# Optimization experiments

Hardware: AMD Instinct MI355X
Metric: run time of the kernel (lower is better)

## Reference

```python
import jax, jax.numpy as jnp
import numpy as np

HIDDEN = 1024
NUM_HEADS = 16
HEAD_DIM = HIDDEN // NUM_HEADS  # 64
MLP_HIDDEN = 4096
RMS_EPS = 1e-6


def setup_inputs() -> dict:
    key = jax.random.key(0)
    ks = jax.random.split(key, 4)
    B, L = 2, 2048
    x = jax.random.normal(ks[0], (B, L, HIDDEN), dtype=jnp.float32)
    pe = jax.random.normal(ks[1], (1, 1, L, HEAD_DIM // 2, 2, 2), dtype=jnp.float32)
    W1 = jax.random.normal(ks[2], (HIDDEN, 3 * HIDDEN + MLP_HIDDEN), dtype=jnp.float32) * (HIDDEN ** -0.5)
    b1 = jnp.zeros((3 * HIDDEN + MLP_HIDDEN,), dtype=jnp.float32)
    W2 = jax.random.normal(ks[3], (HIDDEN + MLP_HIDDEN, HIDDEN), dtype=jnp.float32) * ((HIDDEN + MLP_HIDDEN) ** -0.5)
    b2 = jnp.zeros((HIDDEN,), dtype=jnp.float32)
    q_scale = jnp.ones((HEAD_DIM,), dtype=jnp.float32)
    k_scale = jnp.ones((HEAD_DIM,), dtype=jnp.float32)
    return {"x": x, "pe": pe, "W1": W1, "b1": b1, "W2": W2, "b2": b2,
            "q_scale": q_scale, "k_scale": k_scale}


def _rms_norm(t, scale):
    # RMSNorm over last dim (head_dim) with learnable scale (flux QKNorm)
    rrms = jax.lax.rsqrt(jnp.mean(jnp.square(t), axis=-1, keepdims=True) + RMS_EPS)
    return t * rrms * scale


def _apply_rope(xq, xk, pe):
    # pe: [1,1,L,D/2,2,2]; x*: [B,H,L,D]
    def rope(t):
        t_ = t.reshape(*t.shape[:-1], -1, 1, 2)  # [B,H,L,D/2,1,2]
        out = pe[..., 0] * t_[..., 0] + pe[..., 1] * t_[..., 1]  # [B,H,L,D/2,2]
        return out.reshape(*t.shape)
    return rope(xq), rope(xk)


def reference(x, pe, W1, b1, W2, b2, q_scale, k_scale):
    B, L, _ = x.shape
    h = x @ W1 + b1  # [B,L,3H+Mh]
    qkv, mlp = h[..., : 3 * HIDDEN], h[..., 3 * HIDDEN:]
    # 'B L (K H D) -> K B H L D'
    qkv = qkv.reshape(B, L, 3, NUM_HEADS, HEAD_DIM).transpose(2, 0, 3, 1, 4)
    q, k, v = qkv[0], qkv[1], qkv[2]
    q = _rms_norm(q, q_scale)
    k = _rms_norm(k, k_scale)
    q, k = _apply_rope(q, k, pe)
    scale = HEAD_DIM ** -0.5
    scores = jnp.einsum('bhqd,bhkd->bhqk', q, k) * scale
    attn = jnp.einsum('bhqk,bhkd->bhqd', jax.nn.softmax(scores, axis=-1), v)
    attn = attn.transpose(0, 2, 1, 3).reshape(B, L, HIDDEN)  # 'B H L D -> B L (H D)'
    out = jnp.concatenate((attn, jax.nn.gelu(mlp)), axis=2) @ W2 + b2
    return out
```

## Files before the change

kernel.cpp:

```cpp
#include <hip/hip_runtime.h>

typedef __bf16 bf16;
typedef __bf16 bf16x8 __attribute__((ext_vector_type(8)));
typedef float f32x4 __attribute__((ext_vector_type(4)));
typedef float f32x16 __attribute__((ext_vector_type(16)));

#define GLDS16(gp, lp) __builtin_amdgcn_global_load_lds( \
    (__attribute__((address_space(1))) void*)(gp), \
    (__attribute__((address_space(3))) void*)(lp), 16, 0, 0)

__device__ inline float ex2(float x) { return exp2f(x); }

__device__ inline float gelu_fast(float x) {
    float t = ex2(-2.3022081702f * (x + 0.044715f * x * x * x));
    return x * __builtin_amdgcn_rcpf(1.0f + t);
}


__global__ void f2b_kernel(const float* __restrict__ src, bf16* __restrict__ dst, long n) {
    long i = ((long)blockIdx.x * 256 + threadIdx.x) * 4;
    if (i + 3 < n) {
        float4 v = *(const float4*)&src[i];
        dst[i + 0] = (bf16)v.x;
        dst[i + 1] = (bf16)v.y;
        dst[i + 2] = (bf16)v.z;
        dst[i + 3] = (bf16)v.w;
    }
}

__global__ __launch_bounds__(256) void transpose_f2b(const float* __restrict__ W,
                                                     bf16* __restrict__ WT,
                                                     int K, int N) {
    __shared__ float tile[32][33];
    int tx = threadIdx.x & 31;
    int ty = threadIdx.x >> 5;
    int n0 = blockIdx.x * 32;
    int k0 = blockIdx.y * 32;
#pragma unroll
    for (int i = 0; i < 4; ++i)
        tile[ty + i * 8][tx] = W[(long)(k0 + ty + i * 8) * N + n0 + tx];
    __syncthreads();
#pragma unroll
    for (int i = 0; i < 4; ++i)
        WT[(long)(n0 + ty + i * 8) * K + k0 + tx] = (bf16)tile[tx][ty + i * 8];
}

template <int EPI>
__global__ __launch_bounds__(256) void gemm_bt(const bf16* __restrict__ A,
                                               const bf16* __restrict__ BT,
                                               const float* __restrict__ bias,
                                               void* __restrict__ C0,
                                               void* __restrict__ C1,
                                               int M, int N, int K, int kch) {
    __shared__ bf16 Asm[128 * 32];
    __shared__ bf16 Bsm[128 * 32];
    int tid = threadIdx.x;
    int w = tid >> 6, l = tid & 63;
    int wr = w >> 1, wc = w & 1;
    int bm = blockIdx.x * 128;
    int bn = blockIdx.y * 128;
    int k0base = (EPI == 1) ? blockIdx.z * kch : 0;

    f32x4 acc[4][4] = {};

    int arow = l >> 2;
    int acol = (l & 3) * 8;
    int fr = l & 15;
    int fk = (l >> 4) * 8;

    int nk = kch >> 5;
    for (int kt = 0; kt < nk; ++kt) {
        int k0 = k0base + kt * 32;
#pragma unroll
        for (int it = 0; it < 2; ++it) {
            int c = it * 4 + w;
            const bf16* ga = A + (long)(bm + c * 16 + arow) * K + k0 + acol;
            GLDS16(ga, &Asm[c * 512]);
            const bf16* gb = BT + (long)(bn + c * 16 + arow) * K + k0 + acol;
            GLDS16(gb, &Bsm[c * 512]);
        }
        asm volatile("s_waitcnt vmcnt(0)" ::: "memory");
        __syncthreads();

        bf16x8 af[4], bfr[4];
#pragma unroll
        for (int m = 0; m < 4; ++m)
            af[m] = *(const bf16x8*)&Asm[(wr * 64 + m * 16 + fr) * 32 + fk];
#pragma unroll
        for (int n = 0; n < 4; ++n)
            bfr[n] = *(const bf16x8*)&Bsm[(wc * 64 + n * 16 + fr) * 32 + fk];
#pragma unroll
        for (int m = 0; m < 4; ++m)
#pragma unroll
            for (int n = 0; n < 4; ++n)
                acc[m][n] = __builtin_amdgcn_mfma_f32_16x16x32_bf16(af[m], bfr[n], acc[m][n], 0, 0, 0);
        __syncthreads();
    }

    int orow0 = bm + wr * 64;
    int ocol0 = bn + wc * 64;
    if (EPI == 0) {
        bf16* hp = (bf16*)C0;
        bf16* cat = (bf16*)C1;
        bool gel = (bn >= 3072);
#pragma unroll
        for (int m = 0; m < 4; ++m) {
            int row = orow0 + m * 16 + (l >> 4) * 4;
#pragma unroll
            for (int n = 0; n < 4; ++n) {
                int col = ocol0 + n * 16 + (l & 15);
                float bv = bias[col];
#pragma unroll
                for (int r = 0; r < 4; ++r) {
                    float v = acc[m][n][r] + bv;
                    if (gel) {
                        cat[(long)(row + r) * 5120 + 1024 + col - 3072] = (bf16)gelu_fast(v);
                    } else {
                        hp[(long)(row + r) * N + col] = (bf16)v;
                    }
                }
            }
        }
    } else {
        float* cz = (float*)C0 + (long)blockIdx.z * M * N;
#pragma unroll
        for (int m = 0; m < 4; ++m) {
            int row = orow0 + m * 16 + (l >> 4) * 4;
#pragma unroll
            for (int n = 0; n < 4; ++n) {
                int col = ocol0 + n * 16 + (l & 15);
#pragma unroll
                for (int r = 0; r < 4; ++r)
                    cz[(long)(row + r) * N + col] = acc[m][n][r];
            }
        }
    }
}

__global__ __launch_bounds__(256) void reduce4_kernel(const float* __restrict__ part,
                                                      const float* __restrict__ b2,
                                                      float* __restrict__ out) {
    const long stride4 = 4096L * 1024 / 4;
#pragma unroll
    for (int it = 0; it < 2; ++it) {
        long i4 = (long)blockIdx.x * 512 + it * 256 + threadIdx.x;
        float4 s = *(const float4*)&b2[(i4 * 4) & 1023];
        const float4* p = (const float4*)part;
#pragma unroll
        for (int z = 0; z < 4; ++z) {
            float4 v = p[z * stride4 + i4];
            s.x += v.x; s.y += v.y; s.z += v.z; s.w += v.w;
        }
        *(float4*)&out[i4 * 4] = s;
    }
}

__global__ __launch_bounds__(256) void qkv_kernel(const bf16* __restrict__ h,
                                                  const float* __restrict__ pe,
                                                  const float* __restrict__ qsc_,
                                                  const float* __restrict__ ksc_,
                                                  bf16* __restrict__ qo,
                                                  bf16* __restrict__ ko) {
    int t = blockIdx.x;
    int b = t >> 11;
    int lpos = t & 2047;
    int wv = threadIdx.x >> 6;
    int d = threadIdx.x & 63;
    const bf16* hrow = h + (long)t * 7168;
    float pe0 = pe[lpos * 128 + (d >> 1) * 4 + (d & 1) * 2 + 0];
    float pe1 = pe[lpos * 128 + (d >> 1) * 4 + (d & 1) * 2 + 1];
    float qsc = qsc_[d], ksc = ksc_[d];
#pragma unroll 1
    for (int it = 0; it < 4; ++it) {
        int hh = wv * 4 + it;
        float qv = (float)hrow[hh * 64 + d];
        float kv = (float)hrow[1024 + hh * 64 + d];
        float ssq = qv * qv, ssk = kv * kv;
#pragma unroll
        for (int off = 1; off < 64; off <<= 1) {
            ssq += __shfl_xor(ssq, off, 64);
            ssk += __shfl_xor(ssk, off, 64);
        }
        float qn = qv * rsqrtf(ssq * (1.0f / 64.0f) + 1e-6f) * qsc;
        float kn = kv * rsqrtf(ssk * (1.0f / 64.0f) + 1e-6f) * ksc;
        float qe = __shfl(qn, d & 62, 64), qodd = __shfl(qn, d | 1, 64);
        float ke = __shfl(kn, d & 62, 64), kodd = __shfl(kn, d | 1, 64);
        float qr = (pe0 * qe + pe1 * qodd) * 0.18033688011112042f;
        float kr = pe0 * ke + pe1 * kodd;
        long base = ((long)(b * 16 + hh) * 2048 + lpos) * 64 + d;
        qo[base] = (bf16)qr;
        ko[base] = (bf16)kr;
    }
}

__global__ __launch_bounds__(256) void vtrans_kernel(const bf16* __restrict__ h,
                                                     bf16* __restrict__ vT) {
    __shared__ unsigned short tile[64 * 65];
    int bh = blockIdx.x;
    int b = bh >> 4, hh = bh & 15;
    int l0 = blockIdx.y * 64;
    int tid = threadIdx.x;

    int r = tid >> 3, c = tid & 7;
#pragma unroll
    for (int p = 0; p < 2; ++p) {
        int row = r + p * 32;
        const bf16* src = h + (long)(b * 2048 + l0 + row) * 7168 + 2048 + hh * 64 + c * 8;
        bf16x8 v = *(const bf16x8*)src;
        union { bf16x8 v; unsigned short s[8]; } u; u.v = v;
#pragma unroll
        for (int e = 0; e < 8; ++e) tile[row * 65 + c * 8 + e] = u.s[e];
    }
    __syncthreads();
#pragma unroll
    for (int p = 0; p < 2; ++p) {
        int idx = tid + p * 256;
        int d = idx >> 3, kg = idx & 7;
        union { bf16x8 v; unsigned short s[8]; } u;
#pragma unroll
        for (int e = 0; e < 8; ++e) u.s[e] = tile[(kg * 8 + e) * 65 + d];
        *(bf16x8*)&vT[((long)bh * 64 + d) * 2048 + l0 + kg * 8] = u.v;
    }
}

__global__ __launch_bounds__(512) void attn_kernel(const bf16* __restrict__ qg,
                                                   const bf16* __restrict__ kg_,
                                                   const bf16* __restrict__ vT,
                                                   bf16* __restrict__ cat) {
    __shared__ __align__(16) char lds[65536];
    char* Kl0 = lds;
    char* Kl1 = lds + 8192;
    char* Vl0 = lds + 16384;
    char* Vl1 = lds + 24576;

    int bidx = blockIdx.x;
    int bh = bidx & 31;
    int qblk = bidx >> 5;
    int b = bh >> 4, hh = bh & 15;
    int tid = threadIdx.x;
    int wv = tid >> 6, l = tid & 63;
    int h = l >> 5, ln = l & 31;
    int sw = (ln & 7) << 4;

    char* Pw = lds + 32768 + wv * 4096;

    const bf16* qbase = qg + ((long)bh * 2048 + qblk * 256 + wv * 32 + ln) * 64 + h * 8;
    bf16x8 qf[4];
#pragma unroll
    for (int ds = 0; ds < 4; ++ds) qf[ds] = *(const bf16x8*)(qbase + ds * 16);

    f32x16 Oa0 = {}, Oa1 = {};
    float m = -1e30f, lsum = 0.0f;

    int kr = tid >> 3, kg = tid & 7;
    int swb = (kg * 16) ^ ((kr & 7) << 4);
    const bf16* gK = kg_ + ((long)bh * 2048 + kr) * 64 + kg * 8;
    const bf16* gV = vT + ((long)bh * 64 + kr) * 2048 + kg * 8;

    bf16x8 rk = *(const bf16x8*)gK;
    bf16x8 rv = *(const bf16x8*)gV;
    *(bf16x8*)(Kl0 + kr * 128 + swb) = rk;
    *(bf16x8*)(Vl0 + kr * 128 + swb) = rv;
    __syncthreads();

    int c = 0;
    for (int t = 0; t < 32; ++t) {
        if (t < 31) {
            rk = *(const bf16x8*)(gK + (long)(t + 1) * 4096);
            rv = *(const bf16x8*)(gV + (t + 1) * 64);
        }
        const char* Kc = c ? Kl1 : Kl0;
        const char* Vc = c ? Vl1 : Vl0;

        f32x16 S0 = {}, S1 = {};
        __builtin_amdgcn_s_setprio(1);
#pragma unroll
        for (int ds = 0; ds < 4; ++ds) {
            bf16x8 kf0 = *(const bf16x8*)(Kc + ln * 128 + ((ds * 32 + h * 16) ^ sw));
            bf16x8 kf1 = *(const bf16x8*)(Kc + (32 + ln) * 128 + ((ds * 32 + h * 16) ^ sw));
            S0 = __builtin_amdgcn_mfma_f32_32x32x16_bf16(kf0, qf[ds], S0, 0, 0, 0);
            S1 = __builtin_amdgcn_mfma_f32_32x32x16_bf16(kf1, qf[ds], S1, 0, 0, 0);
        }
        __builtin_amdgcn_s_setprio(0);

        float tmax = S0[0];
#pragma unroll
        for (int r = 1; r < 16; ++r) tmax = fmaxf(tmax, S0[r]);
#pragma unroll
        for (int r = 0; r < 16; ++r) tmax = fmaxf(tmax, S1[r]);
        tmax = fmaxf(tmax, __shfl_xor(tmax, 32, 64));

        if (!__all(tmax - m <= 8.0f)) {
            float mn = fmaxf(m, tmax);
            float es = ex2(m - mn);
            lsum *= es;
            m = mn;
#pragma unroll
            for (int r = 0; r < 16; ++r) {
                int rowq = (r & 3) + 8 * (r >> 2) + 4 * h;
                float esr = __shfl(es, rowq, 64);
                Oa0[r] *= esr;
                Oa1[r] *= esr;
            }
        }

        float ps = 0.0f;
#pragma unroll
        for (int kvt = 0; kvt < 2; ++kvt) {
            float p[16];
#pragma unroll
            for (int r = 0; r < 16; ++r) {
                float v = ex2((kvt ? S1[r] : S0[r]) - m);
                p[r] = v;
                ps += v;
            }
#pragma unroll
            for (int i = 0; i < 8; ++i) {
                union { bf16 bb[2]; unsigned u; } pr;
                pr.bb[0] = (bf16)p[2 * i];
                pr.bb[1] = (bf16)p[2 * i + 1];
                int kv = ((2 * i) & 3) + 8 * (i >> 1) + 4 * h + 32 * kvt;
                *(unsigned*)(Pw + ln * 128 + ((kv * 2) ^ sw)) = pr.u;
            }
        }
        lsum += ps + __shfl_xor(ps, 32, 64);

        asm volatile("s_waitcnt lgkmcnt(0)" ::: "memory");

        bf16x8 pa[4];
#pragma unroll
        for (int s = 0; s < 4; ++s)
            pa[s] = *(const bf16x8*)(Pw + ln * 128 + ((s * 32 + h * 16) ^ sw));

        __builtin_amdgcn_s_setprio(1);
#pragma unroll
        for (int s = 0; s < 4; ++s) {
            bf16x8 vf0 = *(const bf16x8*)(Vc + ln * 128 + ((s * 32 + h * 16) ^ sw));
            bf16x8 vf1 = *(const bf16x8*)(Vc + (32 + ln) * 128 + ((s * 32 + h * 16) ^ sw));
            Oa0 = __builtin_amdgcn_mfma_f32_32x32x16_bf16(pa[s], vf0, Oa0, 0, 0, 0);
            Oa1 = __builtin_amdgcn_mfma_f32_32x32x16_bf16(pa[s], vf1, Oa1, 0, 0, 0);
        }
        __builtin_amdgcn_s_setprio(0);

        __syncthreads();
        if (t < 31) {
            char* Kn = c ? Kl0 : Kl1;
            char* Vn = c ? Vl0 : Vl1;
            *(bf16x8*)(Kn + kr * 128 + swb) = rk;
            *(bf16x8*)(Vn + kr * 128 + swb) = rv;
        }
        __syncthreads();
        c ^= 1;
    }

#pragma unroll
    for (int r = 0; r < 16; ++r) {
        int rowq = (r & 3) + 8 * (r >> 2) + 4 * h;
        float ls = __shfl(lsum, rowq, 64);
        float inv = 1.0f / ls;
        long trow = (long)b * 2048 + qblk * 256 + wv * 32 + rowq;
        cat[trow * 5120 + hh * 64 + ln] = (bf16)(Oa0[r] * inv);
        cat[trow * 5120 + hh * 64 + 32 + ln] = (bf16)(Oa1[r] * inv);
    }
}


extern "C" void kernel_launch(void* const* d_in, const int* in_sizes, int n_in,
                              void* d_out, int out_size, void* d_ws, size_t ws_size,
                              hipStream_t stream) {
    const float* x  = (const float*)d_in[0];
    const float* pe = (const float*)d_in[1];
    const float* W1 = (const float*)d_in[2];
    const float* b1 = (const float*)d_in[3];
    const float* W2 = (const float*)d_in[4];
    const float* b2 = (const float*)d_in[5];
    const float* qs = (const float*)d_in[6];
    const float* ks = (const float*)d_in[7];
    float* out = (float*)d_out;

    char* ws = (char*)d_ws;
    bf16* xb  = (bf16*)(ws);
    bf16* w1t = (bf16*)(ws + 8388608);
    bf16* w2t = (bf16*)(ws + 23068672);
    bf16* h   = (bf16*)(ws + 33554432);
    bf16* qb  = (bf16*)(ws + 92274688);
    bf16* kb  = (bf16*)(ws + 100663296);
    bf16* vT  = (bf16*)(ws + 109051904);
    bf16* cat = (bf16*)(ws + 117440512);
    float* part = (float*)(ws + 33554432);

    f2b_kernel<<<4096, 256, 0, stream>>>(x, xb, 4194304L);
    transpose_f2b<<<dim3(224, 32), 256, 0, stream>>>(W1, w1t, 1024, 7168);
    transpose_f2b<<<dim3(32, 160), 256, 0, stream>>>(W2, w2t, 5120, 1024);

    gemm_bt<0><<<dim3(32, 56), 256, 0, stream>>>(xb, w1t, b1, h, cat, 4096, 7168, 1024, 1024);

    qkv_kernel<<<4096, 256, 0, stream>>>(h, pe, qs, ks, qb, kb);
    vtrans_kernel<<<dim3(32, 32), 256, 0, stream>>>(h, vT);

    attn_kernel<<<256, 512, 0, stream>>>(qb, kb, vT, cat);

    gemm_bt<1><<<dim3(32, 8, 4), 256, 0, stream>>>(cat, w2t, nullptr, part, nullptr, 4096, 1024, 5120, 1280);
    reduce4_kernel<<<2048, 256, 0, stream>>>(part, b2, out);
}
```

Baseline: 293.3 us.

## Deepen GEMM K-tile to 64 with swizzled LDS and shrink attention blocks

```diff
diff --git a/kernel.cpp b/kernel.cpp
--- a/kernel.cpp
+++ b/kernel.cpp
@@ -52,8 +52,8 @@
                                                void* __restrict__ C0,
                                                void* __restrict__ C1,
                                                int M, int N, int K, int kch) {
-    __shared__ bf16 Asm[128 * 32];
-    __shared__ bf16 Bsm[128 * 32];
+    __shared__ __align__(16) char Asm[128 * 128];
+    __shared__ __align__(16) char Bsm[128 * 128];
     int tid = threadIdx.x;
     int w = tid >> 6, l = tid & 63;
     int wr = w >> 1, wc = w & 1;
@@ -63,37 +63,43 @@
 
     f32x4 acc[4][4] = {};
 
-    int arow = l >> 2;
-    int acol = (l & 3) * 8;
     int fr = l & 15;
-    int fk = (l >> 4) * 8;
-
-    int nk = kch >> 5;
+    int g16 = (l >> 4) * 16;
+    int xsw = (fr & 7) << 4;
+
+    int srow = tid >> 3;
+    int sg8 = ((tid & 7) ^ (srow & 7)) * 8;
+    int dstoff = (w << 10) + ((l & 63) << 4);
+
+    int nk = kch >> 6;
     for (int kt = 0; kt < nk; ++kt) {
-        int k0 = k0base + kt * 32;
-#pragma unroll
-        for (int it = 0; it < 2; ++it) {
-            int c = it * 4 + w;
-            const bf16* ga = A + (long)(bm + c * 16 + arow) * K + k0 + acol;
-            GLDS16(ga, &Asm[c * 512]);
-            const bf16* gb = BT + (long)(bn + c * 16 + arow) * K + k0 + acol;
-            GLDS16(gb, &Bsm[c * 512]);
+        int k0 = k0base + kt * 64;
+#pragma unroll
+        for (int gg = 0; gg < 4; ++gg) {
+            const bf16* ga = A + (long)(bm + gg * 32 + srow) * K + k0 + sg8;
+            GLDS16(ga, Asm + gg * 4096 + dstoff);
+            const bf16* gb = BT + (long)(bn + gg * 32 + srow) * K + k0 + sg8;
+            GLDS16(gb, Bsm + gg * 4096 + dstoff);
         }
         asm volatile("s_waitcnt vmcnt(0)" ::: "memory");
         __syncthreads();
 
-        bf16x8 af[4], bfr[4];
-#pragma unroll
-        for (int m = 0; m < 4; ++m)
-            af[m] = *(const bf16x8*)&Asm[(wr * 64 + m * 16 + fr) * 32 + fk];
-#pragma unroll
-        for (int n = 0; n < 4; ++n)
-            bfr[n] = *(const bf16x8*)&Bsm[(wc * 64 + n * 16 + fr) * 32 + fk];
-#pragma unroll
-        for (int m = 0; m < 4; ++m)
+#pragma unroll
+        for (int kk = 0; kk < 2; ++kk) {
+            int koff = (kk * 64 + g16) ^ xsw;
+            bf16x8 af[4], bfr[4];
+#pragma unroll
+            for (int m = 0; m < 4; ++m)
+                af[m] = *(const bf16x8*)(Asm + (wr * 64 + m * 16 + fr) * 128 + koff);
 #pragma unroll
             for (int n = 0; n < 4; ++n)
-                acc[m][n] = __builtin_amdgcn_mfma_f32_16x16x32_bf16(af[m], bfr[n], acc[m][n], 0, 0, 0);
+                bfr[n] = *(const bf16x8*)(Bsm + (wc * 64 + n * 16 + fr) * 128 + koff);
+#pragma unroll
+            for (int m = 0; m < 4; ++m)
+#pragma unroll
+                for (int n = 0; n < 4; ++n)
+                    acc[m][n] = __builtin_amdgcn_mfma_f32_16x16x32_bf16(af[m], bfr[n], acc[m][n], 0, 0, 0);
+        }
         __syncthreads();
     }
 
@@ -108,7 +114,7 @@
             int row = orow0 + m * 16 + (l >> 4) * 4;
 #pragma unroll
             for (int n = 0; n < 4; ++n) {
-                int col = ocol0 + n * 16 + (l & 15);
+                int col = ocol0 + n * 16 + fr;
                 float bv = bias[col];
 #pragma unroll
                 for (int r = 0; r < 4; ++r) {
@@ -128,7 +134,7 @@
             int row = orow0 + m * 16 + (l >> 4) * 4;
 #pragma unroll
             for (int n = 0; n < 4; ++n) {
-                int col = ocol0 + n * 16 + (l & 15);
+                int col = ocol0 + n * 16 + fr;
 #pragma unroll
                 for (int r = 0; r < 4; ++r)
                     cz[(long)(row + r) * N + col] = acc[m][n][r];
@@ -223,11 +229,11 @@
     }
 }
 
-__global__ __launch_bounds__(512) void attn_kernel(const bf16* __restrict__ qg,
+__global__ __launch_bounds__(256) void attn_kernel(const bf16* __restrict__ qg,
                                                    const bf16* __restrict__ kg_,
                                                    const bf16* __restrict__ vT,
                                                    bf16* __restrict__ cat) {
-    __shared__ __align__(16) char lds[65536];
+    __shared__ __align__(16) char lds[49152];
     char* Kl0 = lds;
     char* Kl1 = lds + 8192;
     char* Vl0 = lds + 16384;
@@ -244,7 +250,7 @@
 
     char* Pw = lds + 32768 + wv * 4096;
 
-    const bf16* qbase = qg + ((long)bh * 2048 + qblk * 256 + wv * 32 + ln) * 64 + h * 8;
+    const bf16* qbase = qg + ((long)bh * 2048 + qblk * 128 + wv * 32 + ln) * 64 + h * 8;
     bf16x8 qf[4];
 #pragma unroll
     for (int ds = 0; ds < 4; ++ds) qf[ds] = *(const bf16x8*)(qbase + ds * 16);
@@ -257,17 +263,23 @@
     const bf16* gK = kg_ + ((long)bh * 2048 + kr) * 64 + kg * 8;
     const bf16* gV = vT + ((long)bh * 64 + kr) * 2048 + kg * 8;
 
-    bf16x8 rk = *(const bf16x8*)gK;
-    bf16x8 rv = *(const bf16x8*)gV;
-    *(bf16x8*)(Kl0 + kr * 128 + swb) = rk;
-    *(bf16x8*)(Vl0 + kr * 128 + swb) = rv;
+    bf16x8 rk0 = *(const bf16x8*)gK;
+    bf16x8 rk1 = *(const bf16x8*)(gK + 32 * 64);
+    bf16x8 rv0 = *(const bf16x8*)gV;
+    bf16x8 rv1 = *(const bf16x8*)(gV + 32 * 2048);
+    *(bf16x8*)(Kl0 + kr * 128 + swb) = rk0;
+    *(bf16x8*)(Kl0 + (kr + 32) * 128 + swb) = rk1;
+    *(bf16x8*)(Vl0 + kr * 128 + swb) = rv0;
+    *(bf16x8*)(Vl0 + (kr + 32) * 128 + swb) = rv1;
     __syncthreads();
 
     int c = 0;
     for (int t = 0; t < 32; ++t) {
         if (t < 31) {
-            rk = *(const bf16x8*)(gK + (long)(t + 1) * 4096);
-            rv = *(const bf16x8*)(gV + (t + 1) * 64);
+            rk0 = *(const bf16x8*)(gK + (long)(t + 1) * 4096);
+            rk1 = *(const bf16x8*)(gK + (long)(t + 1) * 4096 + 32 * 64);
+            rv0 = *(const bf16x8*)(gV + (t + 1) * 64);
+            rv1 = *(const bf16x8*)(gV + (t + 1) * 64 + 32 * 2048);
         }
         const char* Kc = c ? Kl1 : Kl0;
         const char* Vc = c ? Vl1 : Vl0;
@@ -346,8 +358,10 @@
         if (t < 31) {
             char* Kn = c ? Kl0 : Kl1;
             char* Vn = c ? Vl0 : Vl1;
-            *(bf16x8*)(Kn + kr * 128 + swb) = rk;
-            *(bf16x8*)(Vn + kr * 128 + swb) = rv;
+            *(bf16x8*)(Kn + kr * 128 + swb) = rk0;
+            *(bf16x8*)(Kn + (kr + 32) * 128 + swb) = rk1;
+            *(bf16x8*)(Vn + kr * 128 + swb) = rv0;
+            *(bf16x8*)(Vn + (kr + 32) * 128 + swb) = rv1;
         }
         __syncthreads();
         c ^= 1;
@@ -358,7 +372,7 @@
         int rowq = (r & 3) + 8 * (r >> 2) + 4 * h;
         float ls = __shfl(lsum, rowq, 64);
         float inv = 1.0f / ls;
-        long trow = (long)b * 2048 + qblk * 256 + wv * 32 + rowq;
+        long trow = (long)b * 2048 + qblk * 128 + wv * 32 + rowq;
         cat[trow * 5120 + hh * 64 + ln] = (bf16)(Oa0[r] * inv);
         cat[trow * 5120 + hh * 64 + 32 + ln] = (bf16)(Oa1[r] * inv);
     }
@@ -398,7 +412,7 @@
     qkv_kernel<<<4096, 256, 0, stream>>>(h, pe, qs, ks, qb, kb);
     vtrans_kernel<<<dim3(32, 32), 256, 0, stream>>>(h, vT);
 
-    attn_kernel<<<256, 512, 0, stream>>>(qb, kb, vT, cat);
+    attn_kernel<<<512, 256, 0, stream>>>(qb, kb, vT, cat);
 
     gemm_bt<1><<<dim3(32, 8, 4), 256, 0, stream>>>(cat, w2t, nullptr, part, nullptr, 4096, 1024, 5120, 1280);
     reduce4_kernel<<<2048, 256, 0, stream>>>(part, b2, out);
```

Result: faster. 273.8 us (-6.6%).
